# Performance work log

Hardware: AMD Instinct MI355X
Metric: run time of the kernel (lower is better)

The kernel has to match this reference:

```python
import jax, jax.numpy as jnp
import numpy as np

B = 262144  # batch of configurations
J = 24      # revolute joints in a serial chain (base -> link_1 -> ... -> link_J)


def setup_inputs() -> dict:
    key = jax.random.key(0)
    k1, k2, k3, k4 = jax.random.split(key, 4)
    joint_angles = jax.random.normal(k1, (B, J), dtype=jnp.float32)
    xyz = jax.random.uniform(k2, (J, 3), dtype=jnp.float32) * 0.2          # joint origin translation
    rpy = jax.random.uniform(k3, (J, 3), dtype=jnp.float32) * 0.5          # joint origin fixed euler
    axis = jax.random.uniform(k4, (J, 3), dtype=jnp.float32) + 0.1        # revolute axis (unnormalized, as in URDF)
    return {"joint_angles": joint_angles, "xyz": xyz, "rpy": rpy, "axis": axis}


def _euler_to_rot(rpy):
    # (J,3) -> (J,3,3), Rz(y) @ Ry(p) @ Rx(r)
    r, p, y = rpy[:, 0], rpy[:, 1], rpy[:, 2]
    cr, sr = jnp.cos(r), jnp.sin(r)
    cp, sp = jnp.cos(p), jnp.sin(p)
    cy, sy = jnp.cos(y), jnp.sin(y)
    row0 = jnp.stack([cy * cp, cy * sp * sr - sy * cr, cy * sp * cr + sy * sr], -1)
    row1 = jnp.stack([sy * cp, sy * sp * sr + cy * cr, sy * sp * cr - cy * sr], -1)
    row2 = jnp.stack([-sp, cp * sr, cp * cr], -1)
    return jnp.stack([row0, row1, row2], -2)


def _rodrigues(aa):
    # (B,3) axis-angle -> (B,3,3). R = ca*I + (1-ca)*kk^T + sa*[k]_x
    angle = jnp.linalg.norm(aa, axis=-1)
    k = aa / jnp.maximum(angle, 1e-6)[:, None]
    ca, sa = jnp.cos(angle), jnp.sin(angle)
    oc = 1.0 - ca
    kx, ky, kz = k[:, 0], k[:, 1], k[:, 2]
    row0 = jnp.stack([ca + kx * kx * oc, kx * ky * oc - kz * sa, kx * kz * oc + ky * sa], -1)
    row1 = jnp.stack([ky * kx * oc + kz * sa, ca + ky * ky * oc, ky * kz * oc - kx * sa], -1)
    row2 = jnp.stack([kz * kx * oc - ky * sa, kz * ky * oc + kx * sa, ca + kz * kz * oc], -1)
    R = jnp.stack([row0, row1, row2], -2)
    eye = jnp.eye(3, dtype=aa.dtype)
    return jnp.where((angle == 0.0)[:, None, None], eye, R)


def reference(joint_angles, xyz, rpy, axis):
    bs, nj = joint_angles.shape
    dt = joint_angles.dtype
    # fixed per-joint origin transforms (J,4,4)
    Ro = _euler_to_rot(rpy)
    T_origin = (jnp.zeros((nj, 4, 4), dt)
                .at[:, :3, :3].set(Ro)
                .at[:, :3, 3].set(xyz)
                .at[:, 3, 3].set(1.0))

    def step(T_parent, per_joint):
        To, ax, theta = per_joint  # (4,4), (3,), (B,)
        R = _rodrigues(ax[None, :] * theta[:, None])          # (B,3,3)
        T_joint = (jnp.zeros((bs, 4, 4), dt)
                   .at[:, :3, :3].set(R)
                   .at[:, 3, 3].set(1.0))
        T_mid = jnp.einsum('ij,bjk->bik', To, T_joint)        # T_origin @ T_joint
        T_child = jnp.einsum('bij,bjk->bik', T_parent, T_mid) # chain product
        return T_child, T_child[:, :3, 3]

    T_base = jnp.broadcast_to(jnp.eye(4, dtype=dt), (bs, 4, 4))
    _, pos = jax.lax.scan(step, T_base, (T_origin, axis, joint_angles.T))  # pos: (J,B,3)
    # base link position (identity transform) comes first, as in link_names order
    pos = jnp.concatenate([jnp.zeros((1, bs, 3), dt), pos], axis=0)        # (J+1,B,3)
    return jnp.transpose(pos, (1, 0, 2)).reshape(bs, -1)                   # (B, 3*(J+1))
```

## Files before the change

### kernel.cpp

```cpp
#include <hip/hip_runtime.h>

#define NJ 24
#define BLK 128
#define OUTW 75
#define WROWS 64
#define WBUF (WROWS * OUTW)
#define CPB 2
#define CW 12

__global__ __launch_bounds__(BLK, 2) void fk_main_kernel(
    const float* __restrict__ ang,
    const float* __restrict__ xyz,
    const float* __restrict__ rpy,
    const float* __restrict__ axis,
    float* __restrict__ out)
{
    __shared__ float lcst[NJ * CW];
    __shared__ float buf[(BLK / 64) * WBUF];

    const int tid = threadIdx.x;
    const int wv = tid >> 6, ln = tid & 63;
    float* wbuf = &buf[wv * WBUF];

    const long long chunk0 = (long long)blockIdx.x * CPB;

    const float4* gA = (const float4*)(ang + (chunk0 * BLK + tid) * NJ);
    float4 A0 = gA[0], A1 = gA[1], A2 = gA[2], A3 = gA[3], A4 = gA[4], A5 = gA[5];

    if (tid < NJ) {
        const int j = tid;
        float r = rpy[j*3+0] * 0.5f, p = rpy[j*3+1] * 0.5f, yv = rpy[j*3+2] * 0.5f;
        float sr, cr, sp, cp, sy, cy;
        __sincosf(r, &sr, &cr);
        __sincosf(p, &sp, &cp);
        __sincosf(yv, &sy, &cy);
        float qw = cr*cp*cy + sr*sp*sy;
        float qx = sr*cp*cy - cr*sp*sy;
        float qy = cr*sp*cy + sr*cp*sy;
        float qz = cr*cp*sy - sr*sp*cy;
        float ax = axis[j*3+0], ay = axis[j*3+1], az = axis[j*3+2];
        float n = sqrtf(ax*ax + ay*ay + az*az);
        float inv = 1.0f / fmaxf(n, 1e-6f);
        float ux = ax*inv, uy = ay*inv, uz = az*inv;
        float* c = &lcst[j * CW];
        c[0] = qw; c[1] = qx; c[2] = qy; c[3] = qz;
        c[4] = -(qx*ux + qy*uy + qz*uz);
        c[5] = qw*ux + qy*uz - qz*uy;
        c[6] = qw*uy + qz*ux - qx*uz;
        c[7] = qw*uz + qx*uy - qy*ux;
        c[8] = xyz[j*3+0]; c[9] = xyz[j*3+1]; c[10] = xyz[j*3+2];
        c[11] = n * 0.5f;
    }
    __syncthreads();

    #pragma unroll
    for (int c = 0; c < CPB; ++c) {
        float th[NJ] = {A0.x,A0.y,A0.z,A0.w, A1.x,A1.y,A1.z,A1.w,
                        A2.x,A2.y,A2.z,A2.w, A3.x,A3.y,A3.z,A3.w,
                        A4.x,A4.y,A4.z,A4.w, A5.x,A5.y,A5.z,A5.w};

        if (c) {
            asm volatile("s_waitcnt lgkmcnt(0)" ::: "memory");
            __builtin_amdgcn_sched_barrier(0);
        }

        float Qw = 1.f, Qx = 0.f, Qy = 0.f, Qz = 0.f;
        float t0 = 0.f, t1 = 0.f, t2 = 0.f;
        float* ob = wbuf + ln * OUTW;
        ob[0] = 0.f; ob[1] = 0.f; ob[2] = 0.f;

        #pragma unroll
        for (int j = 0; j < NJ; ++j) {
            const float* cc = &lcst[j * CW];
            float h = th[j] * cc[11];
            float s, cq;
            __sincosf(h, &s, &cq);
            float lw = cq*cc[0] + s*cc[4];
            float lx = cq*cc[1] + s*cc[5];
            float ly = cq*cc[2] + s*cc[6];
            float lz = cq*cc[3] + s*cc[7];
            float vx = cc[8], vy = cc[9], vz = cc[10];
            float px = Qy*vz - Qz*vy + Qw*vx;
            float py = Qz*vx - Qx*vz + Qw*vy;
            float pz = Qx*vy - Qy*vx + Qw*vz;
            t0 += vx + 2.0f*(Qy*pz - Qz*py);
            t1 += vy + 2.0f*(Qz*px - Qx*pz);
            t2 += vz + 2.0f*(Qx*py - Qy*px);
            float nw = Qw*lw - Qx*lx - Qy*ly - Qz*lz;
            float nx = Qw*lx + Qx*lw + Qy*lz - Qz*ly;
            float ny = Qw*ly - Qx*lz + Qy*lw + Qz*lx;
            float nz = Qw*lz + Qx*ly - Qy*lx + Qz*lw;
            Qw = nw; Qx = nx; Qy = ny; Qz = nz;
            ob[3*(j+1)+0] = t0;
            ob[3*(j+1)+1] = t1;
            ob[3*(j+1)+2] = t2;
        }

        if (c + 1 < CPB) {
            const float4* gN = (const float4*)(ang + ((chunk0 + c + 1) * BLK + tid) * NJ);
            A0 = gN[0]; A1 = gN[1]; A2 = gN[2]; A3 = gN[3]; A4 = gN[4]; A5 = gN[5];
        }

        asm volatile("s_waitcnt lgkmcnt(0)" ::: "memory");
        __builtin_amdgcn_sched_barrier(0);

        float4* gO = (float4*)(out + (chunk0 + c) * (BLK * OUTW)) + wv * (WBUF / 4);
        const float4* lb = (const float4*)wbuf;
        #pragma unroll
        for (int k = 0; k < 19; ++k) {
            int i = k * 64 + ln;
            if (i < WBUF / 4) gO[i] = lb[i];
        }
    }
}

extern "C" void kernel_launch(void* const* d_in, const int* in_sizes, int n_in,
                              void* d_out, int out_size, void* d_ws, size_t ws_size,
                              hipStream_t stream) {
    const float* ang  = (const float*)d_in[0];
    const float* xyz  = (const float*)d_in[1];
    const float* rpy  = (const float*)d_in[2];
    const float* axis = (const float*)d_in[3];
    float* out = (float*)d_out;

    const int B = in_sizes[0] / NJ;
    const int grid = B / (BLK * CPB);
    fk_main_kernel<<<grid, BLK, 0, stream>>>(ang, xyz, rpy, axis, out);
}
```

Baseline: 28.58 us.

## Split joint chain across 4 lanes with shuffle-based parallel prefix scan

```diff
diff --git a/kernel.cpp b/kernel.cpp
--- a/kernel.cpp
+++ b/kernel.cpp
@@ -1,14 +1,16 @@
 #include <hip/hip_runtime.h>
 
+typedef float f4 __attribute__((ext_vector_type(4)));
+typedef float f2 __attribute__((ext_vector_type(2)));
+
 #define NJ 24
-#define BLK 128
+#define BLK 256
 #define OUTW 75
-#define WROWS 64
-#define WBUF (WROWS * OUTW)
-#define CPB 2
+#define RPW 16
+#define RPB 64
 #define CW 12
 
-__global__ __launch_bounds__(BLK, 2) void fk_main_kernel(
+__global__ __launch_bounds__(BLK, 5) void fk_main_kernel(
     const float* __restrict__ ang,
     const float* __restrict__ xyz,
     const float* __restrict__ rpy,
@@ -16,23 +18,24 @@
     float* __restrict__ out)
 {
     __shared__ float lcst[NJ * CW];
-    __shared__ float buf[(BLK / 64) * WBUF];
+    __shared__ float buf[RPB * OUTW];
 
     const int tid = threadIdx.x;
     const int wv = tid >> 6, ln = tid & 63;
-    float* wbuf = &buf[wv * WBUF];
+    const int q = ln & 3, r = ln >> 2;
 
-    const long long chunk0 = (long long)blockIdx.x * CPB;
+    const long long row = (long long)blockIdx.x * RPB + wv * RPW + r;
 
-    const float4* gA = (const float4*)(ang + (chunk0 * BLK + tid) * NJ);
-    float4 A0 = gA[0], A1 = gA[1], A2 = gA[2], A3 = gA[3], A4 = gA[4], A5 = gA[5];
+    const f2* ga = (const f2*)(ang + row * NJ + q * 6);
+    f2 a0 = ga[0], a1 = ga[1], a2 = ga[2];
+    float th[6] = {a0.x, a0.y, a1.x, a1.y, a2.x, a2.y};
 
     if (tid < NJ) {
         const int j = tid;
-        float r = rpy[j*3+0] * 0.5f, p = rpy[j*3+1] * 0.5f, yv = rpy[j*3+2] * 0.5f;
+        float rr = rpy[j*3+0] * 0.5f, p = rpy[j*3+1] * 0.5f, yv = rpy[j*3+2] * 0.5f;
         float sr, cr, sp, cp, sy, cy;
-        __sincosf(r, &sr, &cr);
-        __sincosf(p, &sp, &cp);
+        __sincosf(rr, &sr, &cr);
+        __sincosf(p,  &sp, &cp);
         __sincosf(yv, &sy, &cy);
         float qw = cr*cp*cy + sr*sp*sy;
         float qx = sr*cp*cy - cr*sp*sy;
@@ -53,64 +56,90 @@
     }
     __syncthreads();
 
+    float Qw=1.f,Qx=0.f,Qy=0.f,Qz=0.f, t0=0.f,t1=0.f,t2=0.f;
+    float plx[6], ply[6], plz[6];
     #pragma unroll
-    for (int c = 0; c < CPB; ++c) {
-        float th[NJ] = {A0.x,A0.y,A0.z,A0.w, A1.x,A1.y,A1.z,A1.w,
-                        A2.x,A2.y,A2.z,A2.w, A3.x,A3.y,A3.z,A3.w,
-                        A4.x,A4.y,A4.z,A4.w, A5.x,A5.y,A5.z,A5.w};
+    for (int i = 0; i < 6; ++i) {
+        const float* cc = &lcst[(q*6 + i) * CW];
+        float h = th[i] * cc[11];
+        float s, cq;
+        __sincosf(h, &s, &cq);
+        float lw = cq*cc[0] + s*cc[4];
+        float lx = cq*cc[1] + s*cc[5];
+        float ly = cq*cc[2] + s*cc[6];
+        float lz = cq*cc[3] + s*cc[7];
+        float vx = cc[8], vy = cc[9], vz = cc[10];
+        float px = Qy*vz - Qz*vy + Qw*vx;
+        float py = Qz*vx - Qx*vz + Qw*vy;
+        float pz = Qx*vy - Qy*vx + Qw*vz;
+        t0 += vx + 2.f*(Qy*pz - Qz*py);
+        t1 += vy + 2.f*(Qz*px - Qx*pz);
+        t2 += vz + 2.f*(Qx*py - Qy*px);
+        plx[i] = t0; ply[i] = t1; plz[i] = t2;
+        float nw = Qw*lw - Qx*lx - Qy*ly - Qz*lz;
+        float nx = Qw*lx + Qx*lw + Qy*lz - Qz*ly;
+        float ny = Qw*ly - Qx*lz + Qy*lw + Qz*lx;
+        float nz = Qw*lz + Qx*ly - Qy*lx + Qz*lw;
+        Qw = nw; Qx = nx; Qy = ny; Qz = nz;
+    }
 
-        if (c) {
-            asm volatile("s_waitcnt lgkmcnt(0)" ::: "memory");
-            __builtin_amdgcn_sched_barrier(0);
+    float Iw=Qw, Ix=Qx, Iy=Qy, Iz=Qz, It0=t0, It1=t1, It2=t2;
+    #pragma unroll
+    for (int d = 1; d < 4; d <<= 1) {
+        float Jw  = __shfl_up(Iw, d, 4);
+        float Jx  = __shfl_up(Ix, d, 4);
+        float Jy  = __shfl_up(Iy, d, 4);
+        float Jz  = __shfl_up(Iz, d, 4);
+        float Jt0 = __shfl_up(It0, d, 4);
+        float Jt1 = __shfl_up(It1, d, 4);
+        float Jt2 = __shfl_up(It2, d, 4);
+        if (q >= d) {
+            float px = Jy*It2 - Jz*It1 + Jw*It0;
+            float py = Jz*It0 - Jx*It2 + Jw*It1;
+            float pz = Jx*It1 - Jy*It0 + Jw*It2;
+            float r0 = It0 + 2.f*(Jy*pz - Jz*py);
+            float r1 = It1 + 2.f*(Jz*px - Jx*pz);
+            float r2 = It2 + 2.f*(Jx*py - Jy*px);
+            It0 = Jt0 + r0; It1 = Jt1 + r1; It2 = Jt2 + r2;
+            float nw = Jw*Iw - Jx*Ix - Jy*Iy - Jz*Iz;
+            float nx = Jw*Ix + Jx*Iw + Jy*Iz - Jz*Iy;
+            float ny = Jw*Iy - Jx*Iz + Jy*Iw + Jz*Ix;
+            float nz = Jw*Iz + Jx*Iy - Jy*Ix + Jz*Iw;
+            Iw = nw; Ix = nx; Iy = ny; Iz = nz;
         }
+    }
+    float Pw  = __shfl_up(Iw, 1, 4);
+    float Px  = __shfl_up(Ix, 1, 4);
+    float Py  = __shfl_up(Iy, 1, 4);
+    float Pz  = __shfl_up(Iz, 1, 4);
+    float Pt0 = __shfl_up(It0, 1, 4);
+    float Pt1 = __shfl_up(It1, 1, 4);
+    float Pt2 = __shfl_up(It2, 1, 4);
+    if (q == 0) { Pw = 1.f; Px = 0.f; Py = 0.f; Pz = 0.f;
+                  Pt0 = 0.f; Pt1 = 0.f; Pt2 = 0.f; }
 
-        float Qw = 1.f, Qx = 0.f, Qy = 0.f, Qz = 0.f;
-        float t0 = 0.f, t1 = 0.f, t2 = 0.f;
-        float* ob = wbuf + ln * OUTW;
-        ob[0] = 0.f; ob[1] = 0.f; ob[2] = 0.f;
+    float* ob = &buf[(wv * RPW + r) * OUTW];
+    if (q == 0) { ob[0] = 0.f; ob[1] = 0.f; ob[2] = 0.f; }
+    #pragma unroll
+    for (int i = 0; i < 6; ++i) {
+        float vx = plx[i], vy = ply[i], vz = plz[i];
+        float px = Py*vz - Pz*vy + Pw*vx;
+        float py = Pz*vx - Px*vz + Pw*vy;
+        float pz = Px*vy - Py*vx + Pw*vz;
+        int c = (q*6 + i + 1) * 3;
+        ob[c+0] = Pt0 + vx + 2.f*(Py*pz - Pz*py);
+        ob[c+1] = Pt1 + vy + 2.f*(Pz*px - Px*pz);
+        ob[c+2] = Pt2 + vz + 2.f*(Px*py - Py*px);
+    }
 
-        #pragma unroll
-        for (int j = 0; j < NJ; ++j) {
-            const float* cc = &lcst[j * CW];
-            float h = th[j] * cc[11];
-            float s, cq;
-            __sincosf(h, &s, &cq);
-            float lw = cq*cc[0] + s*cc[4];
-            float lx = cq*cc[1] + s*cc[5];
-            float ly = cq*cc[2] + s*cc[6];
-            float lz = cq*cc[3] + s*cc[7];
-            float vx = cc[8], vy = cc[9], vz = cc[10];
-            float px = Qy*vz - Qz*vy + Qw*vx;
-            float py = Qz*vx - Qx*vz + Qw*vy;
-            float pz = Qx*vy - Qy*vx + Qw*vz;
-            t0 += vx + 2.0f*(Qy*pz - Qz*py);
-            t1 += vy + 2.0f*(Qz*px - Qx*pz);
-            t2 += vz + 2.0f*(Qx*py - Qy*px);
-            float nw = Qw*lw - Qx*lx - Qy*ly - Qz*lz;
-            float nx = Qw*lx + Qx*lw + Qy*lz - Qz*ly;
-            float ny = Qw*ly - Qx*lz + Qy*lw + Qz*lx;
-            float nz = Qw*lz + Qx*ly - Qy*lx + Qz*lw;
-            Qw = nw; Qx = nx; Qy = ny; Qz = nz;
-            ob[3*(j+1)+0] = t0;
-            ob[3*(j+1)+1] = t1;
-            ob[3*(j+1)+2] = t2;
-        }
+    asm volatile("" ::: "memory");
 
-        if (c + 1 < CPB) {
-            const float4* gN = (const float4*)(ang + ((chunk0 + c + 1) * BLK + tid) * NJ);
-            A0 = gN[0]; A1 = gN[1]; A2 = gN[2]; A3 = gN[3]; A4 = gN[4]; A5 = gN[5];
-        }
-
-        asm volatile("s_waitcnt lgkmcnt(0)" ::: "memory");
-        __builtin_amdgcn_sched_barrier(0);
-
-        float4* gO = (float4*)(out + (chunk0 + c) * (BLK * OUTW)) + wv * (WBUF / 4);
-        const float4* lb = (const float4*)wbuf;
-        #pragma unroll
-        for (int k = 0; k < 19; ++k) {
-            int i = k * 64 + ln;
-            if (i < WBUF / 4) gO[i] = lb[i];
-        }
+    const f4* lb = (const f4*)&buf[wv * RPW * OUTW];
+    f4* gO = (f4*)(out + (long long)blockIdx.x * (RPB * OUTW) + wv * (RPW * OUTW));
+    #pragma unroll
+    for (int k = 0; k < 5; ++k) {
+        int i = k * 64 + ln;
+        if (i < (RPW * OUTW) / 4) gO[i] = lb[i];
     }
 }
 
@@ -124,6 +153,6 @@
     float* out = (float*)d_out;
 
     const int B = in_sizes[0] / NJ;
-    const int grid = B / (BLK * CPB);
+    const int grid = B / RPB;
     fk_main_kernel<<<grid, BLK, 0, stream>>>(ang, xyz, rpy, axis, out);
 }
```

After: 106.6 us. +272.9%, slower.
